# Optimization experiments

Measured on AMD Instinct MI355X. Metric: run time of the kernel, lower is better.

The kernel has to match this reference:

```python
import math
import jax, jax.numpy as jnp
import numpy as np

B, N, D = 16384, 16, 2
HIDDEN, DL = 64, 5
OMEGA = 1.0
CUSP_GAMMA = 1.0 / (D - 1)  # dim=2 -> 1.0


def _linear_params(key, fan_in, fan_out):
    kw, kb = jax.random.split(key)
    bound = 1.0 / math.sqrt(fan_in)
    w = jax.random.uniform(kw, (fan_out, fan_in), jnp.float32, -bound, bound)
    b = jax.random.uniform(kb, (fan_out,), jnp.float32, -bound, bound)
    return w, b


def setup_inputs() -> dict:
    key = jax.random.key(0)
    ks = jax.random.split(key, 9)
    x = jax.random.normal(ks[0], (B, N, D), jnp.float32)
    phi_w0, phi_b0 = _linear_params(ks[1], D + 1, HIDDEN)
    phi_w1, phi_b1 = _linear_params(ks[2], HIDDEN, HIDDEN)
    phi_w2, phi_b2 = _linear_params(ks[3], HIDDEN, DL)
    psi_w0, psi_b0 = _linear_params(ks[4], 6, HIDDEN)
    psi_w1, psi_b1 = _linear_params(ks[5], HIDDEN, HIDDEN)
    psi_w2, psi_b2 = _linear_params(ks[6], HIDDEN, DL)
    rho_w0, rho_b0 = _linear_params(ks[7], 2 * DL, HIDDEN)
    # rho output layer: weight std=0.01 normal, bias zeros (matches torch init)
    rho_w1 = 0.01 * jax.random.normal(ks[8], (1, HIDDEN), jnp.float32)
    rho_b1 = jnp.zeros((1,), jnp.float32)
    return dict(x=x,
                phi_w0=phi_w0, phi_b0=phi_b0, phi_w1=phi_w1, phi_b1=phi_b1,
                phi_w2=phi_w2, phi_b2=phi_b2,
                psi_w0=psi_w0, psi_b0=psi_b0, psi_w1=psi_w1, psi_b1=psi_b1,
                psi_w2=psi_w2, psi_b2=psi_b2,
                rho_w0=rho_w0, rho_b0=rho_b0, rho_w1=rho_w1, rho_b1=rho_b1)


def _mlp3(h, w0, b0, w1, b1, w2, b2):
    h = jax.nn.gelu(h @ w0.T + b0, approximate=False)
    h = jax.nn.gelu(h @ w1.T + b1, approximate=False)
    return h @ w2.T + b2


def reference(x, phi_w0, phi_b0, phi_w1, phi_b1, phi_w2, phi_b2,
              psi_w0, psi_b0, psi_w1, psi_b1, psi_w2, psi_b2,
              rho_w0, rho_b0, rho_w1, rho_b1):
    # one-body branch
    xs = x * math.sqrt(OMEGA)                       # [B,N,D]
    r2 = (xs ** 2).sum(-1, keepdims=True)           # [B,N,1]
    phi_in = jnp.concatenate([xs, r2], -1)          # [B,N,D+1]
    phi_out = _mlp3(phi_in, phi_w0, phi_b0, phi_w1, phi_b1, phi_w2, phi_b2).mean(1)  # [B,dL]

    # two-body branch: vectorized over all N*(N-1)/2 pairs
    ii, jj = jnp.triu_indices(N, k=1)               # static pair index lists, P entries
    dr = x[:, ii, :] - x[:, jj, :]                  # [B,P,D]
    rij = jnp.sqrt((dr ** 2).sum(-1) + 1e-12)       # [B,P]
    feat = jnp.stack([jnp.log1p(rij), rij / (1 + rij), jnp.exp(-rij ** 2),
                      jnp.exp(-0.5 * rij), jnp.exp(-rij), jnp.exp(-2 * rij)], -1)  # [B,P,6]
    psi_out = _mlp3(feat, psi_w0, psi_b0, psi_w1, psi_b1, psi_w2, psi_b2).mean(1)  # [B,dL]
    cusp = CUSP_GAMMA * (rij * jnp.exp(-rij)).sum(-1)  # [B]

    # readout
    rho_in = jnp.concatenate([phi_out, psi_out], -1)   # [B,2*dL]
    h = jax.nn.gelu(rho_in @ rho_w0.T + rho_b0, approximate=False)
    f = (h @ rho_w1.T + rho_b1).squeeze(-1)            # [B]
    return f + cusp
```

## Files before the change

### kernel.cpp

```cpp
#include <hip/hip_runtime.h>
#include <hip/hip_bf16.h>
#include <math.h>

#define B_TOT 16384
#define NPART 16
#define NPAIR 120
#define HID   64
#define DL    5
#define GB    4
#define PSI_ROWS 120
#define SF_PHI   480
#define SH_ROWS  72
#define PHI_LOC  56

typedef __attribute__((ext_vector_type(8))) short short8;
typedef __attribute__((ext_vector_type(4))) float floatx4;

#define CSC      2.45556851f
#define INV_CSC  0.40723744f

__device__ __forceinline__ unsigned pk2(float a, float b) {
    unsigned r;
    asm("v_cvt_pk_bf16_f32 %0, %1, %2" : "=v"(r) : "v"(a), "v"(b));
    return r;
}

__device__ __forceinline__ float gelu_pre(float z) {
    float e = __builtin_amdgcn_exp2f(-z);
    return z * __builtin_amdgcn_rcpf(1.0f + e);
}

__device__ __forceinline__ float gelu_sig(float v) {
    float e = __builtin_amdgcn_exp2f(-2.45556851f * v);
    return v * __builtin_amdgcn_rcpf(1.0f + e);
}

__device__ __forceinline__ float wred(float v) {
    v += __shfl_down(v, 32);
    v += __shfl_down(v, 16);
    v += __shfl_down(v, 8);
    v += __shfl_down(v, 4);
    v += __shfl_down(v, 2);
    v += __shfl_down(v, 1);
    return v;
}

__global__ __launch_bounds__(256) void jastrow_mfma15(
    const float* __restrict__ x,
    const float* __restrict__ phi_w0, const float* __restrict__ phi_b0,
    const float* __restrict__ phi_w1, const float* __restrict__ phi_b1,
    const float* __restrict__ phi_w2, const float* __restrict__ phi_b2,
    const float* __restrict__ psi_w0, const float* __restrict__ psi_b0,
    const float* __restrict__ psi_w1, const float* __restrict__ psi_b1,
    const float* __restrict__ psi_w2, const float* __restrict__ psi_b2,
    const float* __restrict__ rho_w0, const float* __restrict__ rho_b0,
    const float* __restrict__ rho_w1, const float* __restrict__ rho_b1,
    float* __restrict__ out)
{
    const int t    = threadIdx.x;
    const int lane = t & 63;
    const int wv   = t >> 6;
    const int q    = lane >> 4;
    const int m15  = lane & 15;
    const int bg   = blockIdx.x * GB;

    __shared__ __align__(16) unsigned short s_h[SH_ROWS * 64];
    __shared__ __align__(16) unsigned char  s_mem[8704];
    __shared__ float s_cusp[GB];

    unsigned short* s_f  = (unsigned short*)s_mem;
    float*          s_cs = (float*)s_mem;

    const float2* x2 = (const float2*)x;
    float cusp = 0.f;

    {
        const int bl = wv;
        {
            int p = lane;
            int u = 119 - p;
            float sq = sqrtf((float)(8 * u + 1));
            int k = (int)((sq - 1.0f) * 0.5f);
            int i = 14 - k;
            int j = p - (i * (31 - i)) / 2 + i + 1;

            float2 xi = x2[(bg + bl) * NPART + i];
            float2 xj = x2[(bg + bl) * NPART + j];
            float dx = xi.x - xj.x, dy = xi.y - xj.y;
            float r = sqrtf(dx * dx + dy * dy + 1e-12f);

            float f0 = 0.69314718056f * __builtin_amdgcn_logf(1.f + r);
            float f1 = r * __builtin_amdgcn_rcpf(1.f + r);
            float f3 = __builtin_amdgcn_exp2f(-0.72134752044f * r);
            float f4 = f3 * f3;
            float f5 = f4 * f4;
            float f2 = __builtin_amdgcn_exp2f(-1.44269504089f * r * r);
            cusp += r * f4;

            union { short8 s; unsigned u4[4]; } v;
            v.u4[0] = pk2(f0, f1);
            v.u4[1] = pk2(f2, f3);
            v.u4[2] = pk2(f4, f5);
            v.u4[3] = 0u;
            *(short8*)&s_f[(bl * PSI_ROWS + p) * 8] = v.s;
        }
        if (lane < NPAIR - 64) {
            int p = 64 + lane;
            int u = 119 - p;
            float sq = sqrtf((float)(8 * u + 1));
            int k = (int)((sq - 1.0f) * 0.5f);
            int i = 14 - k;
            int j = p - (i * (31 - i)) / 2 + i + 1;

            float2 xi = x2[(bg + bl) * NPART + i];
            float2 xj = x2[(bg + bl) * NPART + j];
            float dx = xi.x - xj.x, dy = xi.y - xj.y;
            float r = sqrtf(dx * dx + dy * dy + 1e-12f);

            float f0 = 0.69314718056f * __builtin_amdgcn_logf(1.f + r);
            float f1 = r * __builtin_amdgcn_rcpf(1.f + r);
            float f3 = __builtin_amdgcn_exp2f(-0.72134752044f * r);
            float f4 = f3 * f3;
            float f5 = f4 * f4;
            float f2 = __builtin_amdgcn_exp2f(-1.44269504089f * r * r);
            cusp += r * f4;

            union { short8 s; unsigned u4[4]; } v;
            v.u4[0] = pk2(f0, f1);
            v.u4[1] = pk2(f2, f3);
            v.u4[2] = pk2(f4, f5);
            v.u4[3] = 0u;
            *(short8*)&s_f[(bl * PSI_ROWS + p) * 8] = v.s;
        }
        if (lane >= 48) {
            int n = lane - 48;
            float2 xv = x2[(bg + bl) * NPART + n];
            float r2 = xv.x * xv.x + xv.y * xv.y;
            union { short8 s; unsigned u4[4]; } w;
            w.u4[0] = pk2(xv.x, xv.y);
            w.u4[1] = pk2(r2, 0.f);
            w.u4[2] = 0u; w.u4[3] = 0u;
            *(short8*)&s_f[(SF_PHI + bl * NPART + n) * 8] = w.s;
        }
    }

    const int colb = wv * 16 + m15;
    int swz[4];
#pragma unroll
    for (int rg = 0; rg < 4; ++rg) swz[rg] = colb ^ (((q * 4 + rg) & 7) << 3);

    short8 Bp1 = (short8)0, Bf1 = (short8)0;
    if (q == 0) {
        union { short8 s; unsigned u4[4]; } bb;
        const float* w = psi_w0 + colb * 6;
        bb.u4[0] = pk2(CSC * w[0], CSC * w[1]);
        bb.u4[1] = pk2(CSC * w[2], CSC * w[3]);
        bb.u4[2] = pk2(CSC * w[4], CSC * w[5]);
        bb.u4[3] = 0u;
        Bp1 = bb.s;
        const float* wf = phi_w0 + colb * 3;
        bb.u4[0] = pk2(CSC * wf[0], CSC * wf[1]);
        bb.u4[1] = pk2(CSC * wf[2], 0.f);
        bb.u4[2] = 0u; bb.u4[3] = 0u;
        Bf1 = bb.s;
    }
    float b0p = CSC * psi_b0[colb], b0f = CSC * phi_b0[colb];
    floatx4 C0p = {b0p, b0p, b0p, b0p};
    floatx4 C0f = {b0f, b0f, b0f, b0f};

    short8 Bp2[2], Bf2[2];
#pragma unroll
    for (int Kc = 0; Kc < 2; ++Kc) {
        const floatx4* wp4 = (const floatx4*)(psi_w1 + colb * HID + Kc * 32 + q * 8);
        const floatx4* wf4 = (const floatx4*)(phi_w1 + colb * HID + Kc * 32 + q * 8);
        floatx4 pA = wp4[0], pB = wp4[1];
        floatx4 fA = wf4[0], fB = wf4[1];
        union { short8 s; unsigned u4[4]; } bp, bf;
        bp.u4[0] = pk2(pA[0], pA[1]); bp.u4[1] = pk2(pA[2], pA[3]);
        bp.u4[2] = pk2(pB[0], pB[1]); bp.u4[3] = pk2(pB[2], pB[3]);
        bf.u4[0] = pk2(fA[0], fA[1]); bf.u4[1] = pk2(fA[2], fA[3]);
        bf.u4[2] = pk2(fB[0], fB[1]); bf.u4[3] = pk2(fB[2], fB[3]);
        Bp2[Kc] = bp.s; Bf2[Kc] = bf.s;
    }
    float b1p = CSC * psi_b1[colb], b1f = CSC * phi_b1[colb];
    floatx4 C1p = {b1p, b1p, b1p, b1p};
    floatx4 C1f = {b1f, b1f, b1f, b1f};

    const int g0 = ((q ^ (m15 & 7)) << 3);
    const int g1 = g0 ^ 32;

    float csP[GB] = {0.f, 0.f, 0.f, 0.f};
    float csF[GB] = {0.f, 0.f, 0.f, 0.f};

    __syncthreads();

#pragma unroll
    for (int bl = 0; bl < GB; ++bl) {
#pragma unroll
        for (int Mt = 0; Mt < 4; ++Mt) {
            short8 a = *(const short8*)&s_f[(bl * PSI_ROWS + Mt * 16 + m15) * 8];
            floatx4 d = __builtin_amdgcn_mfma_f32_16x16x32_bf16(a, Bp1, C0p, 0, 0, 0);
            unsigned u01 = pk2(gelu_pre(d[0]), gelu_pre(d[1]));
            unsigned u23 = pk2(gelu_pre(d[2]), gelu_pre(d[3]));
            s_h[(Mt * 16 + q * 4 + 0) * 64 + swz[0]] = (unsigned short)u01;
            s_h[(Mt * 16 + q * 4 + 1) * 64 + swz[1]] = (unsigned short)(u01 >> 16);
            s_h[(Mt * 16 + q * 4 + 2) * 64 + swz[2]] = (unsigned short)u23;
            s_h[(Mt * 16 + q * 4 + 3) * 64 + swz[3]] = (unsigned short)(u23 >> 16);
        }
        __syncthreads();
#pragma unroll
        for (int Mt = 0; Mt < 4; ++Mt) {
            int rb = (Mt * 16 + m15) * 64;
            short8 a0 = *(const short8*)&s_h[rb + g0];
            short8 a1 = *(const short8*)&s_h[rb + g1];
            floatx4 acc = __builtin_amdgcn_mfma_f32_16x16x32_bf16(a0, Bp2[0], C1p, 0, 0, 0);
            acc = __builtin_amdgcn_mfma_f32_16x16x32_bf16(a1, Bp2[1], acc, 0, 0, 0);
#pragma unroll
            for (int rg = 0; rg < 4; ++rg) {
                float z = acc[rg];
                float rr = __builtin_amdgcn_rcpf(1.0f + __builtin_amdgcn_exp2f(-z));
                csP[bl] = __builtin_fmaf(z, rr, csP[bl]);
            }
        }
        __syncthreads();

#pragma unroll
        for (int Mt2 = 0; Mt2 < 4; ++Mt2) {
            const int Mt = 4 + Mt2;
            short8 a = *(const short8*)&s_f[(bl * PSI_ROWS + Mt * 16 + m15) * 8];
            floatx4 d = __builtin_amdgcn_mfma_f32_16x16x32_bf16(a, Bp1, C0p, 0, 0, 0);
            if (Mt2 < 3 || q < 2) {
                unsigned u01 = pk2(gelu_pre(d[0]), gelu_pre(d[1]));
                unsigned u23 = pk2(gelu_pre(d[2]), gelu_pre(d[3]));
                s_h[(Mt2 * 16 + q * 4 + 0) * 64 + swz[0]] = (unsigned short)u01;
                s_h[(Mt2 * 16 + q * 4 + 1) * 64 + swz[1]] = (unsigned short)(u01 >> 16);
                s_h[(Mt2 * 16 + q * 4 + 2) * 64 + swz[2]] = (unsigned short)u23;
                s_h[(Mt2 * 16 + q * 4 + 3) * 64 + swz[3]] = (unsigned short)(u23 >> 16);
            }
        }
        {
            short8 a = *(const short8*)&s_f[(SF_PHI + bl * NPART + m15) * 8];
            floatx4 d = __builtin_amdgcn_mfma_f32_16x16x32_bf16(a, Bf1, C0f, 0, 0, 0);
            unsigned u01 = pk2(gelu_pre(d[0]), gelu_pre(d[1]));
            unsigned u23 = pk2(gelu_pre(d[2]), gelu_pre(d[3]));
            s_h[(PHI_LOC + q * 4 + 0) * 64 + swz[0]] = (unsigned short)u01;
            s_h[(PHI_LOC + q * 4 + 1) * 64 + swz[1]] = (unsigned short)(u01 >> 16);
            s_h[(PHI_LOC + q * 4 + 2) * 64 + swz[2]] = (unsigned short)u23;
            s_h[(PHI_LOC + q * 4 + 3) * 64 + swz[3]] = (unsigned short)(u23 >> 16);
        }
        __syncthreads();
#pragma unroll
        for (int Mt2 = 0; Mt2 < 4; ++Mt2) {
            int rb = (Mt2 * 16 + m15) * 64;
            short8 a0 = *(const short8*)&s_h[rb + g0];
            short8 a1 = *(const short8*)&s_h[rb + g1];
            floatx4 acc = __builtin_amdgcn_mfma_f32_16x16x32_bf16(a0, Bp2[0], C1p, 0, 0, 0);
            acc = __builtin_amdgcn_mfma_f32_16x16x32_bf16(a1, Bp2[1], acc, 0, 0, 0);
            if (Mt2 == 3) {
                if (q < 2) {
#pragma unroll
                    for (int rg = 0; rg < 4; ++rg) {
                        float z = acc[rg];
                        float rr = __builtin_amdgcn_rcpf(1.0f + __builtin_amdgcn_exp2f(-z));
                        csP[bl] = __builtin_fmaf(z, rr, csP[bl]);
                    }
                }
            } else {
#pragma unroll
                for (int rg = 0; rg < 4; ++rg) {
                    float z = acc[rg];
                    float rr = __builtin_amdgcn_rcpf(1.0f + __builtin_amdgcn_exp2f(-z));
                    csP[bl] = __builtin_fmaf(z, rr, csP[bl]);
                }
            }
        }
        {
            int rb = (PHI_LOC + m15) * 64;
            short8 a0 = *(const short8*)&s_h[rb + g0];
            short8 a1 = *(const short8*)&s_h[rb + g1];
            floatx4 acc = __builtin_amdgcn_mfma_f32_16x16x32_bf16(a0, Bf2[0], C1f, 0, 0, 0);
            acc = __builtin_amdgcn_mfma_f32_16x16x32_bf16(a1, Bf2[1], acc, 0, 0, 0);
#pragma unroll
            for (int rg = 0; rg < 4; ++rg) {
                float z = acc[rg];
                float rr = __builtin_amdgcn_rcpf(1.0f + __builtin_amdgcn_exp2f(-z));
                csF[bl] = __builtin_fmaf(z, rr, csF[bl]);
            }
        }
        if (bl < GB - 1) __syncthreads();
    }

#pragma unroll
    for (int bl = 0; bl < GB; ++bl) {
        s_cs[(((0 * GB + bl) * 4 + wv) * 4 + q) * 16 + m15] = csP[bl];
        s_cs[(((1 * GB + bl) * 4 + wv) * 4 + q) * 16 + m15] = csF[bl];
    }
    {
        float cc = wred(cusp);
        if (lane == 0) s_cusp[wv] = cc;
    }
    __syncthreads();

    {
        const int blr = wv;
        const int c   = lane;
        const int cw  = c >> 4, cm = c & 15;
        float colP = 0.f, colF = 0.f;
#pragma unroll
        for (int qq = 0; qq < 4; ++qq) {
            colP += s_cs[(((0 * GB + blr) * 4 + cw) * 4 + qq) * 16 + cm];
            colF += s_cs[(((1 * GB + blr) * 4 + cw) * 4 + qq) * 16 + cm];
        }
        colP *= INV_CSC;
        colF *= INV_CSC;

        float psiv[DL], phiv[DL];
#pragma unroll
        for (int d = 0; d < DL; ++d) {
            float sP = wred(colP * psi_w2[d * HID + c]);
            psiv[d] = __shfl(sP, 0) * (1.0f / NPAIR) + psi_b2[d];
            float sF = wred(colF * phi_w2[d * HID + c]);
            phiv[d] = __shfl(sF, 0) * (1.0f / NPART) + phi_b2[d];
        }

        int j = lane;
        float a = rho_b0[j];
        const float* wr = rho_w0 + j * (2 * DL);
#pragma unroll
        for (int d = 0; d < DL; ++d)
            a += phiv[d] * wr[d] + psiv[d] * wr[DL + d];
        float cuspb = s_cusp[blr];
        float cv = gelu_sig(a) * rho_w1[j];
        cv = wred(cv);
        if (j == 0) out[bg + blr] = cv + rho_b1[0] + cuspb;
    }
}

extern "C" void kernel_launch(void* const* d_in, const int* in_sizes, int n_in,
                              void* d_out, int out_size, void* d_ws, size_t ws_size,
                              hipStream_t stream) {
    const float* x      = (const float*)d_in[0];
    const float* phi_w0 = (const float*)d_in[1];
    const float* phi_b0 = (const float*)d_in[2];
    const float* phi_w1 = (const float*)d_in[3];
    const float* phi_b1 = (const float*)d_in[4];
    const float* phi_w2 = (const float*)d_in[5];
    const float* phi_b2 = (const float*)d_in[6];
    const float* psi_w0 = (const float*)d_in[7];
    const float* psi_b0 = (const float*)d_in[8];
    const float* psi_w1 = (const float*)d_in[9];
    const float* psi_b1 = (const float*)d_in[10];
    const float* psi_w2 = (const float*)d_in[11];
    const float* psi_b2 = (const float*)d_in[12];
    const float* rho_w0 = (const float*)d_in[13];
    const float* rho_b0 = (const float*)d_in[14];
    const float* rho_w1 = (const float*)d_in[15];
    const float* rho_b1 = (const float*)d_in[16];

    jastrow_mfma15<<<B_TOT / GB, 256, 0, stream>>>(
        x,
        phi_w0, phi_b0, phi_w1, phi_b1, phi_w2, phi_b2,
        psi_w0, psi_b0, psi_w1, psi_b1, psi_w2, psi_b2,
        rho_w0, rho_b0, rho_w1, rho_b1,
        (float*)d_out);
}
```

Baseline: 164.7 us.

## Double-buffer hidden activations to overlap layer-1 and layer-2 MFMA phases

Splits the hidden-activation scratch into two halves so that the layer-2 MFMA of one chunk runs alongside the layer-1 MFMA of the next chunk. This software-pipelines the per-sample loop and cuts the barriers from four to two per sample. Shared memory for the hidden buffer grows from 72 to 136 rows, which may lower occupancy.

```diff
diff --git a/kernel.cpp b/kernel.cpp
--- a/kernel.cpp
+++ b/kernel.cpp
@@ -10,8 +10,7 @@
 #define GB    4
 #define PSI_ROWS 120
 #define SF_PHI   480
-#define SH_ROWS  72
-#define PHI_LOC  56
+#define CHB      64
 
 typedef __attribute__((ext_vector_type(8))) short short8;
 typedef __attribute__((ext_vector_type(4))) float floatx4;
@@ -45,7 +44,7 @@
     return v;
 }
 
-__global__ __launch_bounds__(256) void jastrow_mfma15(
+__global__ __launch_bounds__(256) void jastrow_mfma19(
     const float* __restrict__ x,
     const float* __restrict__ phi_w0, const float* __restrict__ phi_b0,
     const float* __restrict__ phi_w1, const float* __restrict__ phi_b1,
@@ -64,7 +63,7 @@
     const int m15  = lane & 15;
     const int bg   = blockIdx.x * GB;
 
-    __shared__ __align__(16) unsigned short s_h[SH_ROWS * 64];
+    __shared__ __align__(16) unsigned short s_h[136 * 64];
     __shared__ __align__(16) unsigned char  s_mem[8704];
     __shared__ float s_cusp[GB];
 
@@ -192,10 +191,7 @@
     float csP[GB] = {0.f, 0.f, 0.f, 0.f};
     float csF[GB] = {0.f, 0.f, 0.f, 0.f};
 
-    __syncthreads();
-
-#pragma unroll
-    for (int bl = 0; bl < GB; ++bl) {
+    auto PH1A = [&](int bl) {
 #pragma unroll
         for (int Mt = 0; Mt < 4; ++Mt) {
             short8 a = *(const short8*)&s_f[(bl * PSI_ROWS + Mt * 16 + m15) * 8];
@@ -207,23 +203,8 @@
             s_h[(Mt * 16 + q * 4 + 2) * 64 + swz[2]] = (unsigned short)u23;
             s_h[(Mt * 16 + q * 4 + 3) * 64 + swz[3]] = (unsigned short)(u23 >> 16);
         }
-        __syncthreads();
-#pragma unroll
-        for (int Mt = 0; Mt < 4; ++Mt) {
-            int rb = (Mt * 16 + m15) * 64;
-            short8 a0 = *(const short8*)&s_h[rb + g0];
-            short8 a1 = *(const short8*)&s_h[rb + g1];
-            floatx4 acc = __builtin_amdgcn_mfma_f32_16x16x32_bf16(a0, Bp2[0], C1p, 0, 0, 0);
-            acc = __builtin_amdgcn_mfma_f32_16x16x32_bf16(a1, Bp2[1], acc, 0, 0, 0);
-#pragma unroll
-            for (int rg = 0; rg < 4; ++rg) {
-                float z = acc[rg];
-                float rr = __builtin_amdgcn_rcpf(1.0f + __builtin_amdgcn_exp2f(-z));
-                csP[bl] = __builtin_fmaf(z, rr, csP[bl]);
-            }
-        }
-        __syncthreads();
-
+    };
+    auto PH1B = [&](int bl) {
 #pragma unroll
         for (int Mt2 = 0; Mt2 < 4; ++Mt2) {
             const int Mt = 4 + Mt2;
@@ -232,10 +213,10 @@
             if (Mt2 < 3 || q < 2) {
                 unsigned u01 = pk2(gelu_pre(d[0]), gelu_pre(d[1]));
                 unsigned u23 = pk2(gelu_pre(d[2]), gelu_pre(d[3]));
-                s_h[(Mt2 * 16 + q * 4 + 0) * 64 + swz[0]] = (unsigned short)u01;
-                s_h[(Mt2 * 16 + q * 4 + 1) * 64 + swz[1]] = (unsigned short)(u01 >> 16);
-                s_h[(Mt2 * 16 + q * 4 + 2) * 64 + swz[2]] = (unsigned short)u23;
-                s_h[(Mt2 * 16 + q * 4 + 3) * 64 + swz[3]] = (unsigned short)(u23 >> 16);
+                s_h[(CHB + Mt2 * 16 + q * 4 + 0) * 64 + swz[0]] = (unsigned short)u01;
+                s_h[(CHB + Mt2 * 16 + q * 4 + 1) * 64 + swz[1]] = (unsigned short)(u01 >> 16);
+                s_h[(CHB + Mt2 * 16 + q * 4 + 2) * 64 + swz[2]] = (unsigned short)u23;
+                s_h[(CHB + Mt2 * 16 + q * 4 + 3) * 64 + swz[3]] = (unsigned short)(u23 >> 16);
             }
         }
         {
@@ -243,15 +224,32 @@
             floatx4 d = __builtin_amdgcn_mfma_f32_16x16x32_bf16(a, Bf1, C0f, 0, 0, 0);
             unsigned u01 = pk2(gelu_pre(d[0]), gelu_pre(d[1]));
             unsigned u23 = pk2(gelu_pre(d[2]), gelu_pre(d[3]));
-            s_h[(PHI_LOC + q * 4 + 0) * 64 + swz[0]] = (unsigned short)u01;
-            s_h[(PHI_LOC + q * 4 + 1) * 64 + swz[1]] = (unsigned short)(u01 >> 16);
-            s_h[(PHI_LOC + q * 4 + 2) * 64 + swz[2]] = (unsigned short)u23;
-            s_h[(PHI_LOC + q * 4 + 3) * 64 + swz[3]] = (unsigned short)(u23 >> 16);
-        }
-        __syncthreads();
+            s_h[(CHB + 56 + q * 4 + 0) * 64 + swz[0]] = (unsigned short)u01;
+            s_h[(CHB + 56 + q * 4 + 1) * 64 + swz[1]] = (unsigned short)(u01 >> 16);
+            s_h[(CHB + 56 + q * 4 + 2) * 64 + swz[2]] = (unsigned short)u23;
+            s_h[(CHB + 56 + q * 4 + 3) * 64 + swz[3]] = (unsigned short)(u23 >> 16);
+        }
+    };
+    auto PH2A = [&](int bl) {
+#pragma unroll
+        for (int Mt = 0; Mt < 4; ++Mt) {
+            int rb = (Mt * 16 + m15) * 64;
+            short8 a0 = *(const short8*)&s_h[rb + g0];
+            short8 a1 = *(const short8*)&s_h[rb + g1];
+            floatx4 acc = __builtin_amdgcn_mfma_f32_16x16x32_bf16(a0, Bp2[0], C1p, 0, 0, 0);
+            acc = __builtin_amdgcn_mfma_f32_16x16x32_bf16(a1, Bp2[1], acc, 0, 0, 0);
+#pragma unroll
+            for (int rg = 0; rg < 4; ++rg) {
+                float z = acc[rg];
+                float rr = __builtin_amdgcn_rcpf(1.0f + __builtin_amdgcn_exp2f(-z));
+                csP[bl] = __builtin_fmaf(z, rr, csP[bl]);
+            }
+        }
+    };
+    auto PH2B = [&](int bl) {
 #pragma unroll
         for (int Mt2 = 0; Mt2 < 4; ++Mt2) {
-            int rb = (Mt2 * 16 + m15) * 64;
+            int rb = (CHB + Mt2 * 16 + m15) * 64;
             short8 a0 = *(const short8*)&s_h[rb + g0];
             short8 a1 = *(const short8*)&s_h[rb + g1];
             floatx4 acc = __builtin_amdgcn_mfma_f32_16x16x32_bf16(a0, Bp2[0], C1p, 0, 0, 0);
@@ -275,7 +273,7 @@
             }
         }
         {
-            int rb = (PHI_LOC + m15) * 64;
+            int rb = (CHB + 56 + m15) * 64;
             short8 a0 = *(const short8*)&s_h[rb + g0];
             short8 a1 = *(const short8*)&s_h[rb + g1];
             floatx4 acc = __builtin_amdgcn_mfma_f32_16x16x32_bf16(a0, Bf2[0], C1f, 0, 0, 0);
@@ -287,7 +285,22 @@
                 csF[bl] = __builtin_fmaf(z, rr, csF[bl]);
             }
         }
-        if (bl < GB - 1) __syncthreads();
+    };
+
+    __syncthreads();
+    PH1A(0);
+    __syncthreads();
+
+#pragma unroll
+    for (int bl = 0; bl < GB; ++bl) {
+        PH2A(bl);
+        PH1B(bl);
+        __syncthreads();
+        PH2B(bl);
+        if (bl < GB - 1) {
+            PH1A(bl + 1);
+            __syncthreads();
+        }
     }
 
 #pragma unroll
@@ -357,7 +370,7 @@
     const float* rho_w1 = (const float*)d_in[15];
     const float* rho_b1 = (const float*)d_in[16];
 
-    jastrow_mfma15<<<B_TOT / GB, 256, 0, stream>>>(
+    jastrow_mfma19<<<B_TOT / GB, 256, 0, stream>>>(
         x,
         phi_w0, phi_b0, phi_w1, phi_b1, phi_w2, phi_b2,
         psi_w0, psi_b0, psi_w1, psi_b1, psi_w2, psi_b2,
```

Measured after the change: 170.1 us. 3.3% more time.
